# Kernel optimization log

Measured on AMD Instinct MI355X. Metric: run time of the kernel, lower is better.

Reference implementation:

```python
import jax, jax.numpy as jnp
import numpy as np

N, E = 50000, 800000
D_IN, D_DEG, D_H, D_UP = 96, 32, 256, 128
EPS = 0.0  # non-trainable buffer, initial_eps=0


def setup_inputs() -> dict:
    key = jax.random.key(0)
    ks = jax.random.split(key, 8)
    d = D_IN + D_DEG  # 128, feature dim after degree-as-tag concat
    return {
        "x": jax.random.normal(ks[0], (N, D_IN), dtype=jnp.float32),
        "degrees": jax.random.uniform(ks[1], (N, D_DEG), dtype=jnp.float32),
        "edge_features": jax.random.normal(ks[2], (E, d), dtype=jnp.float32),
        "W1": jax.random.normal(ks[3], (d, D_H), dtype=jnp.float32) * (1.0 / np.sqrt(d)),
        "b1": jnp.zeros((D_H,), dtype=jnp.float32),
        "W2": jax.random.normal(ks[4], (D_H, D_UP), dtype=jnp.float32) * (1.0 / np.sqrt(D_H)),
        "b2": jnp.zeros((D_UP,), dtype=jnp.float32),
        "edge_index": jax.random.randint(ks[5], (2, E), 0, N, dtype=jnp.int64),
    }


def reference(x, degrees, edge_features, W1, b1, W2, b2, edge_index):
    # degree_as_tag + retain_features: concat node features with degree tags
    h = jnp.concatenate([x, degrees], axis=-1)  # [N, 128]
    # flow='source_to_target': source j = edge_index[0], target i = edge_index[1]
    src, dst = edge_index[0], edge_index[1]
    msgs = jax.nn.relu(h[src] + edge_features)  # [E, 128]
    agg = jax.ops.segment_sum(msgs, dst, num_segments=N)  # [N, 128]
    z = (1.0 + EPS) * h + agg
    # update MLP: Linear -> ReLU -> Linear
    out = jax.nn.relu(z @ W1 + b1) @ W2 + b2  # [N, 128]
    return out
```

## Files before the change

### kernel.cpp

```cpp
#include <hip/hip_runtime.h>


constexpr int DIN  = 96;
constexpr int DDEG = 32;
constexpr int D    = 128;
constexpr int DH   = 256;
constexpr int DUP  = 128;

typedef short bf16x8 __attribute__((ext_vector_type(8)));
typedef float f32x4  __attribute__((ext_vector_type(4)));
typedef unsigned short u16x4 __attribute__((ext_vector_type(4)));

static __device__ __forceinline__ ushort f2bf(float f) {
    unsigned u = __float_as_uint(f);
    unsigned r = (u + 0x7fff + ((u >> 16) & 1)) >> 16;
    return (ushort)r;
}
static __device__ __forceinline__ float4 bfv_to_f4(u16x4 u) {
    float4 r;
    r.x = __uint_as_float((unsigned)u.x << 16);
    r.y = __uint_as_float((unsigned)u.y << 16);
    r.z = __uint_as_float((unsigned)u.z << 16);
    r.w = __uint_as_float((unsigned)u.w << 16);
    return r;
}

static __device__ __forceinline__ int waveInclScan(int v, int lane) {
#pragma unroll
    for (int off = 1; off < 64; off <<= 1) {
        int t = __shfl_up(v, off, 64);
        if (lane >= off) v += t;
    }
    return v;
}

__global__ __launch_bounds__(256) void init_h_kernel(
    const float* __restrict__ x, const float* __restrict__ deg,
    const float* __restrict__ W1, const float* __restrict__ W2,
    ushort* __restrict__ hp, ushort* __restrict__ w1p, ushort* __restrict__ w2p,
    int* __restrict__ counts, int N) {
    int t = blockIdx.x * 256 + threadIdx.x;
    if (t < (N >> 2)) *reinterpret_cast<int4*>(&counts[t * 4]) = make_int4(0, 0, 0, 0);
    if (t == (N >> 2) && (N & 3)) {
        for (int i = (N & ~3); i < N; ++i) counts[i] = 0;
    }
    if (t < 32768) {
        {
            int j = t & 7, l = (t >> 3) & 63, nb = (t >> 9) & 15, kb = t >> 13;
            w1p[t] = f2bf(W1[(kb * 32 + (l >> 4) * 8 + j) * DH + nb * 16 + (l & 15)]);
        }
        {
            int j = t & 7, l = (t >> 3) & 63, nb = (t >> 9) & 7, kb = t >> 12;
            w2p[t] = f2bf(W2[(kb * 32 + (l >> 4) * 8 + j) * DUP + nb * 16 + (l & 15)]);
        }
    }
    if (t >= N * 32) return;
    int n = t >> 5, c = t & 31;
    float4 v;
    if (c < 24) v = *reinterpret_cast<const float4*>(&x[(size_t)n * DIN + c * 4]);
    else        v = *reinterpret_cast<const float4*>(&deg[(size_t)n * DDEG + (c - 24) * 4]);
    u16x4 o;
    o.x = f2bf(v.x); o.y = f2bf(v.y); o.z = f2bf(v.z); o.w = f2bf(v.w);
    *reinterpret_cast<u16x4*>(&hp[(size_t)n * D + c * 4]) = o;
}

__global__ __launch_bounds__(256) void count_kernel(
    const int* __restrict__ ei, int* __restrict__ counts, int N, int E) {
    int e = blockIdx.x * 256 + threadIdx.x;
    if (e >= E) return;
    atomicAdd(&counts[ei[E + e]], 1);
}

__global__ __launch_bounds__(256) void scan_partial_kernel(
    const int* __restrict__ counts, int* __restrict__ blockSums, int N) {
    const int tid = threadIdx.x;
    int base = blockIdx.x * 1024 + tid * 4;
    int4 c = make_int4(0, 0, 0, 0);
    if (base + 3 < N) c = *reinterpret_cast<const int4*>(&counts[base]);
    else if (base < N) {
        c.x = counts[base];
        if (base + 1 < N) c.y = counts[base + 1];
        if (base + 2 < N) c.z = counts[base + 2];
    }
    int s = c.x + c.y + c.z + c.w;
#pragma unroll
    for (int off = 32; off; off >>= 1) s += __shfl_xor(s, off, 64);
    __shared__ int wsum[4];
    if ((tid & 63) == 0) wsum[tid >> 6] = s;
    __syncthreads();
    if (tid == 0) blockSums[blockIdx.x] = wsum[0] + wsum[1] + wsum[2] + wsum[3];
}

__global__ __launch_bounds__(64) void scan_base_kernel(
    const int* __restrict__ blockSums, int* __restrict__ blockBase, int nb) {
    int l = threadIdx.x;
    int orig = (l < nb) ? blockSums[l] : 0;
    int incl = waveInclScan(orig, l);
    if (l < nb) blockBase[l] = incl - orig;
}

__global__ __launch_bounds__(256) void scan_final_kernel(
    const int* __restrict__ counts, const int* __restrict__ blockBase,
    int* __restrict__ offsets, int* __restrict__ cursor, int N, int E) {
    const int tid = threadIdx.x, lane = tid & 63, wave = tid >> 6;
    int base = blockIdx.x * 1024 + tid * 4;
    int4 c = make_int4(0, 0, 0, 0);
    if (base + 3 < N) c = *reinterpret_cast<const int4*>(&counts[base]);
    else if (base < N) {
        c.x = counts[base];
        if (base + 1 < N) c.y = counts[base + 1];
        if (base + 2 < N) c.z = counts[base + 2];
    }
    int s = c.x + c.y + c.z + c.w;
    int incl = waveInclScan(s, lane);
    __shared__ int wsum[4];
    if (lane == 63) wsum[wave] = incl;
    __syncthreads();
    int wb = 0;
#pragma unroll
    for (int w = 0; w < 4; ++w)
        if (w < wave) wb += wsum[w];
    int ex = blockBase[blockIdx.x] + wb + (incl - s);
    if (base < N)     { offsets[base]     = ex; cursor[base]     = ex; } ex += c.x;
    if (base + 1 < N) { offsets[base + 1] = ex; cursor[base + 1] = ex; } ex += c.y;
    if (base + 2 < N) { offsets[base + 2] = ex; cursor[base + 2] = ex; } ex += c.z;
    if (base + 3 < N) { offsets[base + 3] = ex; cursor[base + 3] = ex; }
    if (blockIdx.x == 0 && tid == 0) offsets[N] = E;
}

__global__ __launch_bounds__(256) void fill_kernel(
    const int* __restrict__ ei, int* __restrict__ cursor,
    int2* __restrict__ eids2, int E) {
    int e = blockIdx.x * 256 + threadIdx.x;
    if (e >= E) return;
    int src = ei[e];
    int dst = ei[E + e];
    int pos = atomicAdd(&cursor[dst], 1);
    eids2[pos] = make_int2(e, src);
}

__global__ __launch_bounds__(256) void gather_mlp_kernel(
    const ushort* __restrict__ hp, const float* __restrict__ ef,
    const int* __restrict__ offsets, const int2* __restrict__ eids2,
    const ushort* __restrict__ w1p, const float* __restrict__ b1,
    const ushort* __restrict__ w2p, const float* __restrict__ b2,
    float* __restrict__ out, int N) {
    __shared__ ushort zs[64][D];
    __shared__ ushort u_lds[4][16][DH + 8];
    const int tid = threadIdx.x;
    const int m0 = blockIdx.x * 64;

    {
        const int hw = tid >> 5, c = tid & 31;
        for (int i = 0; i < 8; ++i) {
            int nl = hw * 8 + i;
            int node = m0 + nl;
            if (node >= N) break;
            float4 h = bfv_to_f4(*reinterpret_cast<const u16x4*>(&hp[(size_t)node * D + c * 4]));
            float4 acc = make_float4(0.f, 0.f, 0.f, 0.f);
            const int pEnd = offsets[node + 1];
            int p = offsets[node];
            for (; p + 4 <= pEnd; p += 4) {
                int2 i0 = eids2[p + 0];
                int2 i1 = eids2[p + 1];
                int2 i2 = eids2[p + 2];
                int2 i3 = eids2[p + 3];
                f32x4 f0 = __builtin_nontemporal_load(
                    reinterpret_cast<const f32x4*>(&ef[(size_t)i0.x * D + c * 4]));
                f32x4 f1 = __builtin_nontemporal_load(
                    reinterpret_cast<const f32x4*>(&ef[(size_t)i1.x * D + c * 4]));
                f32x4 f2 = __builtin_nontemporal_load(
                    reinterpret_cast<const f32x4*>(&ef[(size_t)i2.x * D + c * 4]));
                f32x4 f3 = __builtin_nontemporal_load(
                    reinterpret_cast<const f32x4*>(&ef[(size_t)i3.x * D + c * 4]));
                float4 h0 = bfv_to_f4(*reinterpret_cast<const u16x4*>(&hp[(size_t)i0.y * D + c * 4]));
                float4 h1 = bfv_to_f4(*reinterpret_cast<const u16x4*>(&hp[(size_t)i1.y * D + c * 4]));
                float4 h2 = bfv_to_f4(*reinterpret_cast<const u16x4*>(&hp[(size_t)i2.y * D + c * 4]));
                float4 h3 = bfv_to_f4(*reinterpret_cast<const u16x4*>(&hp[(size_t)i3.y * D + c * 4]));
                acc.x += fmaxf(f0[0] + h0.x, 0.f) + fmaxf(f1[0] + h1.x, 0.f)
                       + fmaxf(f2[0] + h2.x, 0.f) + fmaxf(f3[0] + h3.x, 0.f);
                acc.y += fmaxf(f0[1] + h0.y, 0.f) + fmaxf(f1[1] + h1.y, 0.f)
                       + fmaxf(f2[1] + h2.y, 0.f) + fmaxf(f3[1] + h3.y, 0.f);
                acc.z += fmaxf(f0[2] + h0.z, 0.f) + fmaxf(f1[2] + h1.z, 0.f)
                       + fmaxf(f2[2] + h2.z, 0.f) + fmaxf(f3[2] + h3.z, 0.f);
                acc.w += fmaxf(f0[3] + h0.w, 0.f) + fmaxf(f1[3] + h1.w, 0.f)
                       + fmaxf(f2[3] + h2.w, 0.f) + fmaxf(f3[3] + h3.w, 0.f);
            }
            for (; p < pEnd; ++p) {
                int2 i0 = eids2[p];
                f32x4 f0 = __builtin_nontemporal_load(
                    reinterpret_cast<const f32x4*>(&ef[(size_t)i0.x * D + c * 4]));
                float4 h0 = bfv_to_f4(*reinterpret_cast<const u16x4*>(&hp[(size_t)i0.y * D + c * 4]));
                acc.x += fmaxf(f0[0] + h0.x, 0.f);
                acc.y += fmaxf(f0[1] + h0.y, 0.f);
                acc.z += fmaxf(f0[2] + h0.z, 0.f);
                acc.w += fmaxf(f0[3] + h0.w, 0.f);
            }
            u16x4 o;
            o.x = f2bf(h.x + acc.x);
            o.y = f2bf(h.y + acc.y);
            o.z = f2bf(h.z + acc.z);
            o.w = f2bf(h.w + acc.w);
            *reinterpret_cast<u16x4*>(&zs[nl][c * 4]) = o;
        }
    }
    __syncthreads();

    const int wave = tid >> 6, lane = tid & 63;
    const int lr = lane & 15, lg = lane >> 4;
    const int m0w = m0 + wave * 16;

    bf16x8 a1[4];
    int lrow = wave * 16 + lr;
    if (m0 + lrow > N - 1) lrow = N - 1 - m0;
#pragma unroll
    for (int kb = 0; kb < 4; ++kb)
        a1[kb] = *reinterpret_cast<const bf16x8*>(&zs[lrow][kb * 32 + lg * 8]);

#pragma unroll
    for (int nb = 0; nb < 16; ++nb) {
        f32x4 c = {0.f, 0.f, 0.f, 0.f};
#pragma unroll
        for (int kb = 0; kb < 4; ++kb) {
            bf16x8 b = *reinterpret_cast<const bf16x8*>(&w1p[((kb * 16 + nb) * 64 + lane) * 8]);
            c = __builtin_amdgcn_mfma_f32_16x16x32_bf16(a1[kb], b, c, 0, 0, 0);
        }
        float bias = b1[nb * 16 + lr];
#pragma unroll
        for (int r = 0; r < 4; ++r) {
            float v = fmaxf(c[r] + bias, 0.f);
            u_lds[wave][lg * 4 + r][nb * 16 + lr] = f2bf(v);
        }
    }
    __syncthreads();

    bf16x8 a2[8];
#pragma unroll
    for (int kb = 0; kb < 8; ++kb)
        a2[kb] = *reinterpret_cast<const bf16x8*>(&u_lds[wave][lr][kb * 32 + lg * 8]);

#pragma unroll
    for (int nb = 0; nb < 8; ++nb) {
        f32x4 c = {0.f, 0.f, 0.f, 0.f};
#pragma unroll
        for (int kb = 0; kb < 8; ++kb) {
            bf16x8 b = *reinterpret_cast<const bf16x8*>(&w2p[((kb * 8 + nb) * 64 + lane) * 8]);
            c = __builtin_amdgcn_mfma_f32_16x16x32_bf16(a2[kb], b, c, 0, 0, 0);
        }
        float bias = b2[nb * 16 + lr];
#pragma unroll
        for (int r = 0; r < 4; ++r) {
            int row = m0w + lg * 4 + r;
            if (row < N) out[(size_t)row * DUP + nb * 16 + lr] = c[r] + bias;
        }
    }
}

extern "C" void kernel_launch(void* const* d_in, const int* in_sizes, int n_in,
                              void* d_out, int out_size, void* d_ws, size_t ws_size,
                              hipStream_t stream) {
    const float* x   = (const float*)d_in[0];
    const float* dg  = (const float*)d_in[1];
    const float* ef  = (const float*)d_in[2];
    const float* W1  = (const float*)d_in[3];
    const float* b1  = (const float*)d_in[4];
    const float* W2  = (const float*)d_in[5];
    const float* b2  = (const float*)d_in[6];
    const int*   ei  = (const int*)d_in[7];
    float* out = (float*)d_out;

    const int N = in_sizes[0] / DIN;
    const int E = in_sizes[7] / 2;

    auto align16 = [](size_t v) { return (v + 15) & ~(size_t)15; };
    char* w = (char*)d_ws;
    ushort* hp      = (ushort*)w;  w += align16((size_t)N * D * 2);
    int*   counts   = (int*)w;     w += align16((size_t)N * 4);
    int*   offsets  = (int*)w;     w += align16((size_t)(N + 1) * 4);
    int*   cursor   = (int*)w;     w += align16((size_t)N * 4);
    int2*  eids2    = (int2*)w;    w += align16((size_t)E * 8);
    int*   blockSums= (int*)w;     w += align16(64 * 4);
    int*   blockBase= (int*)w;     w += align16(64 * 4);
    ushort* w1p     = (ushort*)w;  w += align16((size_t)D * DH * 2);
    ushort* w2p     = (ushort*)w;  w += align16((size_t)DH * DUP * 2);

    const int eb = (E + 255) / 256;
    const int nbScan = (N + 1023) / 1024;

    init_h_kernel<<<(N * 32 + 255) / 256, 256, 0, stream>>>(
        x, dg, W1, W2, hp, w1p, w2p, counts, N);
    count_kernel<<<eb, 256, 0, stream>>>(ei, counts, N, E);
    scan_partial_kernel<<<nbScan, 256, 0, stream>>>(counts, blockSums, N);
    scan_base_kernel<<<1, 64, 0, stream>>>(blockSums, blockBase, nbScan);
    scan_final_kernel<<<nbScan, 256, 0, stream>>>(counts, blockBase, offsets, cursor, N, E);
    fill_kernel<<<eb, 256, 0, stream>>>(ei, cursor, eids2, E);

    gather_mlp_kernel<<<(N + 63) / 64, 256, 0, stream>>>(
        hp, ef, offsets, eids2, w1p, b1, w2p, b2, out, N);
}
```

Baseline: 285.1 us.

## Split fused gather+MLP into separate kernels and fold scan base into final scan

Splits the fused gather-and-MLP kernel into a gather kernel (8 nodes per block, one half-wave per node) that writes bf16 z to a workspace buffer, and a separate MFMA MLP kernel that reads z from global memory. The intent is to give the bandwidth-bound gather many more, smaller blocks for better latency hiding and load balance, instead of each block serially handling 8 nodes per half-wave before the MLP. It also removes the single-block scan_base kernel by having each scan_final block reduce the preceding block sums itself. The cost is an extra round trip of z through global memory (about 12.8 MB) and one more kernel launch.

```diff
diff --git a/kernel.cpp b/kernel.cpp
--- a/kernel.cpp
+++ b/kernel.cpp
@@ -24,7 +24,6 @@
     r.w = __uint_as_float((unsigned)u.w << 16);
     return r;
 }
-
 static __device__ __forceinline__ int waveInclScan(int v, int lane) {
 #pragma unroll
     for (int off = 1; off < 64; off <<= 1) {
@@ -91,18 +90,20 @@
     if (tid == 0) blockSums[blockIdx.x] = wsum[0] + wsum[1] + wsum[2] + wsum[3];
 }
 
-__global__ __launch_bounds__(64) void scan_base_kernel(
-    const int* __restrict__ blockSums, int* __restrict__ blockBase, int nb) {
-    int l = threadIdx.x;
-    int orig = (l < nb) ? blockSums[l] : 0;
-    int incl = waveInclScan(orig, l);
-    if (l < nb) blockBase[l] = incl - orig;
-}
-
 __global__ __launch_bounds__(256) void scan_final_kernel(
-    const int* __restrict__ counts, const int* __restrict__ blockBase,
-    int* __restrict__ offsets, int* __restrict__ cursor, int N, int E) {
+    const int* __restrict__ counts, const int* __restrict__ blockSums,
+    int* __restrict__ offsets, int* __restrict__ cursor, int N, int E, int nbScan) {
     const int tid = threadIdx.x, lane = tid & 63, wave = tid >> 6;
+    __shared__ int sBase;
+    __shared__ int wsum[4];
+
+    if (wave == 0) {
+        int v = (lane < blockIdx.x && lane < nbScan) ? blockSums[lane] : 0;
+#pragma unroll
+        for (int off = 32; off; off >>= 1) v += __shfl_xor(v, off, 64);
+        if (lane == 0) sBase = v;
+    }
+
     int base = blockIdx.x * 1024 + tid * 4;
     int4 c = make_int4(0, 0, 0, 0);
     if (base + 3 < N) c = *reinterpret_cast<const int4*>(&counts[base]);
@@ -113,14 +114,13 @@
     }
     int s = c.x + c.y + c.z + c.w;
     int incl = waveInclScan(s, lane);
-    __shared__ int wsum[4];
     if (lane == 63) wsum[wave] = incl;
     __syncthreads();
     int wb = 0;
 #pragma unroll
     for (int w = 0; w < 4; ++w)
         if (w < wave) wb += wsum[w];
-    int ex = blockBase[blockIdx.x] + wb + (incl - s);
+    int ex = sBase + wb + (incl - s);
     if (base < N)     { offsets[base]     = ex; cursor[base]     = ex; } ex += c.x;
     if (base + 1 < N) { offsets[base + 1] = ex; cursor[base + 1] = ex; } ex += c.y;
     if (base + 2 < N) { offsets[base + 2] = ex; cursor[base + 2] = ex; } ex += c.z;
@@ -139,83 +139,81 @@
     eids2[pos] = make_int2(e, src);
 }
 
-__global__ __launch_bounds__(256) void gather_mlp_kernel(
+__global__ __launch_bounds__(256) void gather_kernel(
     const ushort* __restrict__ hp, const float* __restrict__ ef,
     const int* __restrict__ offsets, const int2* __restrict__ eids2,
+    ushort* __restrict__ zb, int N) {
+    const int node = blockIdx.x * 8 + (threadIdx.x >> 5);
+    if (node >= N) return;
+    const int c = threadIdx.x & 31;
+
+    float4 h = bfv_to_f4(*reinterpret_cast<const u16x4*>(&hp[(size_t)node * D + c * 4]));
+
+    float4 acc = make_float4(0.f, 0.f, 0.f, 0.f);
+    const int pEnd = offsets[node + 1];
+    int p = offsets[node];
+
+    for (; p + 4 <= pEnd; p += 4) {
+        int2 i0 = eids2[p + 0];
+        int2 i1 = eids2[p + 1];
+        int2 i2 = eids2[p + 2];
+        int2 i3 = eids2[p + 3];
+        f32x4 f0 = __builtin_nontemporal_load(
+            reinterpret_cast<const f32x4*>(&ef[(size_t)i0.x * D + c * 4]));
+        f32x4 f1 = __builtin_nontemporal_load(
+            reinterpret_cast<const f32x4*>(&ef[(size_t)i1.x * D + c * 4]));
+        f32x4 f2 = __builtin_nontemporal_load(
+            reinterpret_cast<const f32x4*>(&ef[(size_t)i2.x * D + c * 4]));
+        f32x4 f3 = __builtin_nontemporal_load(
+            reinterpret_cast<const f32x4*>(&ef[(size_t)i3.x * D + c * 4]));
+        float4 h0 = bfv_to_f4(*reinterpret_cast<const u16x4*>(&hp[(size_t)i0.y * D + c * 4]));
+        float4 h1 = bfv_to_f4(*reinterpret_cast<const u16x4*>(&hp[(size_t)i1.y * D + c * 4]));
+        float4 h2 = bfv_to_f4(*reinterpret_cast<const u16x4*>(&hp[(size_t)i2.y * D + c * 4]));
+        float4 h3 = bfv_to_f4(*reinterpret_cast<const u16x4*>(&hp[(size_t)i3.y * D + c * 4]));
+        acc.x += fmaxf(f0[0] + h0.x, 0.f) + fmaxf(f1[0] + h1.x, 0.f)
+               + fmaxf(f2[0] + h2.x, 0.f) + fmaxf(f3[0] + h3.x, 0.f);
+        acc.y += fmaxf(f0[1] + h0.y, 0.f) + fmaxf(f1[1] + h1.y, 0.f)
+               + fmaxf(f2[1] + h2.y, 0.f) + fmaxf(f3[1] + h3.y, 0.f);
+        acc.z += fmaxf(f0[2] + h0.z, 0.f) + fmaxf(f1[2] + h1.z, 0.f)
+               + fmaxf(f2[2] + h2.z, 0.f) + fmaxf(f3[2] + h3.z, 0.f);
+        acc.w += fmaxf(f0[3] + h0.w, 0.f) + fmaxf(f1[3] + h1.w, 0.f)
+               + fmaxf(f2[3] + h2.w, 0.f) + fmaxf(f3[3] + h3.w, 0.f);
+    }
+    for (; p < pEnd; ++p) {
+        int2 i0 = eids2[p];
+        f32x4 f0 = __builtin_nontemporal_load(
+            reinterpret_cast<const f32x4*>(&ef[(size_t)i0.x * D + c * 4]));
+        float4 h0 = bfv_to_f4(*reinterpret_cast<const u16x4*>(&hp[(size_t)i0.y * D + c * 4]));
+        acc.x += fmaxf(f0[0] + h0.x, 0.f);
+        acc.y += fmaxf(f0[1] + h0.y, 0.f);
+        acc.z += fmaxf(f0[2] + h0.z, 0.f);
+        acc.w += fmaxf(f0[3] + h0.w, 0.f);
+    }
+    u16x4 o;
+    o.x = f2bf(h.x + acc.x);
+    o.y = f2bf(h.y + acc.y);
+    o.z = f2bf(h.z + acc.z);
+    o.w = f2bf(h.w + acc.w);
+    *reinterpret_cast<u16x4*>(&zb[(size_t)node * D + c * 4]) = o;
+}
+
+__global__ __launch_bounds__(256) void mlp_mfma_kernel(
+    const ushort* __restrict__ zb,
     const ushort* __restrict__ w1p, const float* __restrict__ b1,
     const ushort* __restrict__ w2p, const float* __restrict__ b2,
     float* __restrict__ out, int N) {
-    __shared__ ushort zs[64][D];
     __shared__ ushort u_lds[4][16][DH + 8];
     const int tid = threadIdx.x;
-    const int m0 = blockIdx.x * 64;
-
-    {
-        const int hw = tid >> 5, c = tid & 31;
-        for (int i = 0; i < 8; ++i) {
-            int nl = hw * 8 + i;
-            int node = m0 + nl;
-            if (node >= N) break;
-            float4 h = bfv_to_f4(*reinterpret_cast<const u16x4*>(&hp[(size_t)node * D + c * 4]));
-            float4 acc = make_float4(0.f, 0.f, 0.f, 0.f);
-            const int pEnd = offsets[node + 1];
-            int p = offsets[node];
-            for (; p + 4 <= pEnd; p += 4) {
-                int2 i0 = eids2[p + 0];
-                int2 i1 = eids2[p + 1];
-                int2 i2 = eids2[p + 2];
-                int2 i3 = eids2[p + 3];
-                f32x4 f0 = __builtin_nontemporal_load(
-                    reinterpret_cast<const f32x4*>(&ef[(size_t)i0.x * D + c * 4]));
-                f32x4 f1 = __builtin_nontemporal_load(
-                    reinterpret_cast<const f32x4*>(&ef[(size_t)i1.x * D + c * 4]));
-                f32x4 f2 = __builtin_nontemporal_load(
-                    reinterpret_cast<const f32x4*>(&ef[(size_t)i2.x * D + c * 4]));
-                f32x4 f3 = __builtin_nontemporal_load(
-                    reinterpret_cast<const f32x4*>(&ef[(size_t)i3.x * D + c * 4]));
-                float4 h0 = bfv_to_f4(*reinterpret_cast<const u16x4*>(&hp[(size_t)i0.y * D + c * 4]));
-                float4 h1 = bfv_to_f4(*reinterpret_cast<const u16x4*>(&hp[(size_t)i1.y * D + c * 4]));
-                float4 h2 = bfv_to_f4(*reinterpret_cast<const u16x4*>(&hp[(size_t)i2.y * D + c * 4]));
-                float4 h3 = bfv_to_f4(*reinterpret_cast<const u16x4*>(&hp[(size_t)i3.y * D + c * 4]));
-                acc.x += fmaxf(f0[0] + h0.x, 0.f) + fmaxf(f1[0] + h1.x, 0.f)
-                       + fmaxf(f2[0] + h2.x, 0.f) + fmaxf(f3[0] + h3.x, 0.f);
-                acc.y += fmaxf(f0[1] + h0.y, 0.f) + fmaxf(f1[1] + h1.y, 0.f)
-                       + fmaxf(f2[1] + h2.y, 0.f) + fmaxf(f3[1] + h3.y, 0.f);
-                acc.z += fmaxf(f0[2] + h0.z, 0.f) + fmaxf(f1[2] + h1.z, 0.f)
-                       + fmaxf(f2[2] + h2.z, 0.f) + fmaxf(f3[2] + h3.z, 0.f);
-                acc.w += fmaxf(f0[3] + h0.w, 0.f) + fmaxf(f1[3] + h1.w, 0.f)
-                       + fmaxf(f2[3] + h2.w, 0.f) + fmaxf(f3[3] + h3.w, 0.f);
-            }
-            for (; p < pEnd; ++p) {
-                int2 i0 = eids2[p];
-                f32x4 f0 = __builtin_nontemporal_load(
-                    reinterpret_cast<const f32x4*>(&ef[(size_t)i0.x * D + c * 4]));
-                float4 h0 = bfv_to_f4(*reinterpret_cast<const u16x4*>(&hp[(size_t)i0.y * D + c * 4]));
-                acc.x += fmaxf(f0[0] + h0.x, 0.f);
-                acc.y += fmaxf(f0[1] + h0.y, 0.f);
-                acc.z += fmaxf(f0[2] + h0.z, 0.f);
-                acc.w += fmaxf(f0[3] + h0.w, 0.f);
-            }
-            u16x4 o;
-            o.x = f2bf(h.x + acc.x);
-            o.y = f2bf(h.y + acc.y);
-            o.z = f2bf(h.z + acc.z);
-            o.w = f2bf(h.w + acc.w);
-            *reinterpret_cast<u16x4*>(&zs[nl][c * 4]) = o;
-        }
-    }
-    __syncthreads();
-
     const int wave = tid >> 6, lane = tid & 63;
+    const int m0 = blockIdx.x * 64 + wave * 16;
     const int lr = lane & 15, lg = lane >> 4;
-    const int m0w = m0 + wave * 16;
 
     bf16x8 a1[4];
-    int lrow = wave * 16 + lr;
-    if (m0 + lrow > N - 1) lrow = N - 1 - m0;
+    int rowA = m0 + lr; if (rowA > N - 1) rowA = N - 1;
+    const ushort* zrow = &zb[(size_t)rowA * D + lg * 8];
 #pragma unroll
     for (int kb = 0; kb < 4; ++kb)
-        a1[kb] = *reinterpret_cast<const bf16x8*>(&zs[lrow][kb * 32 + lg * 8]);
+        a1[kb] = *reinterpret_cast<const bf16x8*>(zrow + kb * 32);
 
 #pragma unroll
     for (int nb = 0; nb < 16; ++nb) {
@@ -250,7 +248,7 @@
         float bias = b2[nb * 16 + lr];
 #pragma unroll
         for (int r = 0; r < 4; ++r) {
-            int row = m0w + lg * 4 + r;
+            int row = m0 + lg * 4 + r;
             if (row < N) out[(size_t)row * DUP + nb * 16 + lr] = c[r] + bias;
         }
     }
@@ -274,13 +272,13 @@
 
     auto align16 = [](size_t v) { return (v + 15) & ~(size_t)15; };
     char* w = (char*)d_ws;
+    ushort* zb      = (ushort*)w;  w += align16((size_t)N * D * 2);
     ushort* hp      = (ushort*)w;  w += align16((size_t)N * D * 2);
     int*   counts   = (int*)w;     w += align16((size_t)N * 4);
     int*   offsets  = (int*)w;     w += align16((size_t)(N + 1) * 4);
     int*   cursor   = (int*)w;     w += align16((size_t)N * 4);
     int2*  eids2    = (int2*)w;    w += align16((size_t)E * 8);
     int*   blockSums= (int*)w;     w += align16(64 * 4);
-    int*   blockBase= (int*)w;     w += align16(64 * 4);
     ushort* w1p     = (ushort*)w;  w += align16((size_t)D * DH * 2);
     ushort* w2p     = (ushort*)w;  w += align16((size_t)DH * DUP * 2);
 
@@ -291,10 +289,10 @@
         x, dg, W1, W2, hp, w1p, w2p, counts, N);
     count_kernel<<<eb, 256, 0, stream>>>(ei, counts, N, E);
     scan_partial_kernel<<<nbScan, 256, 0, stream>>>(counts, blockSums, N);
-    scan_base_kernel<<<1, 64, 0, stream>>>(blockSums, blockBase, nbScan);
-    scan_final_kernel<<<nbScan, 256, 0, stream>>>(counts, blockBase, offsets, cursor, N, E);
+    scan_final_kernel<<<nbScan, 256, 0, stream>>>(counts, blockSums, offsets, cursor, N, E, nbScan);
     fill_kernel<<<eb, 256, 0, stream>>>(ei, cursor, eids2, E);
 
-    gather_mlp_kernel<<<(N + 63) / 64, 256, 0, stream>>>(
-        hp, ef, offsets, eids2, w1p, b1, w2p, b2, out, N);
-}
+    gather_kernel<<<(N + 7) / 8, 256, 0, stream>>>(hp, ef, offsets, eids2, zb, N);
+
+    mlp_mfma_kernel<<<(N + 63) / 64, 256, 0, stream>>>(zb, w1p, b1, w2p, b2, out, N);
+}
```

Measured after the change: 240.1 us, median of 2. -15.8%, faster.
